# Kernel optimization log

Measured on AMD Instinct MI355X. Metric: run time of the kernel, lower is better.

Reference implementation:

```python
import jax, jax.numpy as jnp
import numpy as np

# Static layer configuration (from init_kwargs)
C_IN, H, W = 8, 32, 32
C_OUT, KH, KW = 16, 3, 3
SH, SW = 1, 1
PH, PW = 1, 1
OH = (H + 2 * PH - KH) // SH + 1
OW = (W + 2 * PW - KW) // SW + 1
N_IN = C_IN * H * W      # 8192 input-layer neurons
N_OUT = C_OUT * OH * OW  # 16384 output-layer neurons


def setup_inputs() -> dict:
    key = jax.random.key(0)
    k1, k2, k3, k4 = jax.random.split(key, 4)
    base = jax.random.normal(k1, (C_IN, H, W), dtype=jnp.float32)
    rad = jax.random.uniform(k2, (C_IN, H, W), dtype=jnp.float32)
    return {
        "concrete_lower": base - rad,   # ensure lower <= upper
        "concrete_upper": base + rad,
        "weights": jax.random.normal(k3, (C_OUT, C_IN, KH, KW), dtype=jnp.float32) * 0.1,
        "bias": jax.random.normal(k4, (C_OUT,), dtype=jnp.float32) * 0.1,
    }


def build_abstract_matrix(weights, bias):
    """Vectorized equivalent of _create_conv2d_channel_v0 over all channels.

    Produces M of shape (N_IN+1, N_OUT+1): column (c*OH*OW + i*OW + j) holds the
    affine coefficients (over flattened input neurons, bias in last row) of
    output pixel (c, i, j); last column is the homogeneous [0...0, 1] column.
    """
    idy = jnp.arange(OH)[:, None] * SH - PH + jnp.arange(KH)[None, :]  # (OH, KH)
    idx = jnp.arange(OW)[:, None] * SW - PW + jnp.arange(KW)[None, :]  # (OW, KW)
    valid = (((idy >= 0) & (idy < H))[:, :, None, None]
             & ((idx >= 0) & (idx < W))[None, None, :, :])             # (OH, KH, OW, KW)

    cin = jnp.arange(C_IN)
    # broadcast layout: (C_OUT, C_IN, OH, KH, OW, KW)
    rows = (cin[None, :, None, None, None, None] * (H * W)
            + idy[None, None, :, :, None, None] * W
            + idx[None, None, None, None, :, :])
    oc = jnp.arange(C_OUT)
    cols = (oc[:, None, None, None, None, None] * (OH * OW)
            + jnp.arange(OH)[None, None, :, None, None, None] * OW
            + jnp.arange(OW)[None, None, None, None, :, None])
    vals = weights[:, :, None, :, None, :]  # (C_OUT, C_IN, 1, KH, 1, KW)

    shape = (C_OUT, C_IN, OH, KH, OW, KW)
    rows_b = jnp.broadcast_to(rows, shape).reshape(-1)
    cols_b = jnp.broadcast_to(cols, shape).reshape(-1)
    vals_b = jnp.broadcast_to(vals, shape).reshape(-1)
    valid_b = jnp.broadcast_to(valid[None, None], shape).reshape(-1)
    # padding taps (out of input bounds) -> out-of-range row index, dropped by scatter
    rows_b = jnp.where(valid_b, rows_b, N_IN + 1)

    M = jnp.zeros((N_IN + 1, N_OUT + 1), dtype=jnp.float32)
    M = M.at[rows_b, cols_b].set(vals_b, mode="drop")
    M = M.at[N_IN, :N_OUT].set(jnp.repeat(bias, OH * OW))  # bias row per output pixel
    M = M.at[N_IN, N_OUT].set(1.0)                          # homogeneous corner
    return M


def back_substitute(M, l_in, u_in, lower=True):
    # Interval evaluation of the affine map: positive coeffs pair with one bound,
    # negative with the other; last row of M is the bias.
    Wc = M[:-1, :]
    b = M[-1, :]
    pos = jnp.maximum(Wc, 0.0)
    neg = jnp.minimum(Wc, 0.0)
    if lower:
        return l_in @ pos + u_in @ neg + b
    return u_in @ pos + l_in @ neg + b


def reference(concrete_lower, concrete_upper, weights, bias):
    M = build_abstract_matrix(weights, bias)  # abstract lower == upper for a conv layer
    l = concrete_lower.reshape(-1)
    u = concrete_upper.reshape(-1)
    lo = back_substitute(M, l, u, lower=True)[:N_OUT].reshape(C_OUT, OH, OW)
    hi = back_substitute(M, l, u, lower=False)[:N_OUT].reshape(C_OUT, OH, OW)
    return (lo, hi, M)
```

## Files before the change

kernel.cpp:

```cpp
#include <hip/hip_runtime.h>

#define C_IN  8
#define H     32
#define W     32
#define C_OUT 16
#define KH    3
#define KW    3
#define OH    32
#define OW    32
#define N_IN  (C_IN * H * W)
#define N_OUT (C_OUT * OH * OW)
#define MROWS (N_IN + 1)
#define MCOLS (N_OUT + 1)

__global__ __launch_bounds__(256) void build_M(const float* __restrict__ wts,
                                               const float* __restrict__ bias,
                                               float* __restrict__ M) {
    const int row = blockIdx.x;
    const int t   = threadIdx.x;
    float* __restrict__ Mrow = M + (size_t)row * MCOLS;

    if (row == N_IN) {
        for (int k = 0; k < 16; ++k) {
            float b = bias[k];
            float4 v = make_float4(b, b, b, b);
            *(float4*)(Mrow + 1024 * k + 4 * t) = v;
        }
        if (t == 0) Mrow[N_OUT] = 1.0f;
        return;
    }

    const int p    = (4 - (row & 3)) & 3;
    const int Nf   = (MCOLS - p) >> 2;
    const int tail = MCOLS - p - 4 * Nf;

    if (t < p)    Mrow[t] = 0.0f;
    if (t < tail) Mrow[p + 4 * Nf + t] = 0.0f;

    const float4 z = make_float4(0.0f, 0.0f, 0.0f, 0.0f);
    float* base = Mrow + p;
    #pragma unroll
    for (int k = 0; k < 16; ++k) {
        int idx = k * 256 + t;
        if (idx < Nf) *(float4*)(base + 4 * idx) = z;
    }

    const int cin = row >> 10;
    const int iy  = (row >> 5) & 31;
    const int ix  = row & 31;

    int   scol = -1;
    float wv   = 0.0f;
    if (t < C_OUT * KH * KW) {
        int c   = t / 9;
        int rem = t - 9 * c;
        int kh  = rem / 3;
        int kw  = rem - 3 * kh;
        int i   = iy + 1 - kh;
        int j   = ix + 1 - kw;
        if ((unsigned)i < 32u && (unsigned)j < 32u) {
            scol = c * 1024 + i * 32 + j;
            wv   = wts[c * 72 + cin * 9 + rem];
        }
    }

    __syncthreads();

    if (scol >= 0) Mrow[scol] = wv;
}

__global__ __launch_bounds__(256) void bounds_kernel(const float* __restrict__ l_in,
                                                     const float* __restrict__ u_in,
                                                     const float* __restrict__ wts,
                                                     const float* __restrict__ bias,
                                                     float* __restrict__ out) {
    int tid = blockIdx.x * 256 + threadIdx.x;
    if (tid >= N_OUT) return;
    int c = tid >> 10;
    int i = (tid >> 5) & 31;
    int j = tid & 31;

    float lo = bias[c];
    float hi = lo;

    #pragma unroll
    for (int cin = 0; cin < C_IN; ++cin) {
        #pragma unroll
        for (int kh = 0; kh < KH; ++kh) {
            int iy = i - 1 + kh;
            if ((unsigned)iy >= (unsigned)H) continue;
            #pragma unroll
            for (int kw = 0; kw < KW; ++kw) {
                int ix = j - 1 + kw;
                if ((unsigned)ix >= (unsigned)W) continue;
                float w = wts[c * 72 + cin * 9 + kh * 3 + kw];
                int   r = cin * 1024 + iy * 32 + ix;
                float a = w * l_in[r];
                float b = w * u_in[r];
                lo += fminf(a, b);
                hi += fmaxf(a, b);
            }
        }
    }
    out[tid]         = lo;
    out[N_OUT + tid] = hi;
}

extern "C" void kernel_launch(void* const* d_in, const int* in_sizes, int n_in,
                              void* d_out, int out_size, void* d_ws, size_t ws_size,
                              hipStream_t stream) {
    const float* lower = (const float*)d_in[0];
    const float* upper = (const float*)d_in[1];
    const float* wts   = (const float*)d_in[2];
    const float* bias  = (const float*)d_in[3];

    float* out = (float*)d_out;
    float* M   = out + 2 * N_OUT;

    hipLaunchKernelGGL(bounds_kernel, dim3((N_OUT + 255) / 256), dim3(256), 0, stream,
                       lower, upper, wts, bias, out);
    hipLaunchKernelGGL(build_M, dim3(MROWS), dim3(256), 0, stream, wts, bias, M);
}
```

Before: 571.1 us.

## Fuse bounds and matrix build into one kernel, computing M values in-register

Merges the bounds kernel and the M-construction kernel into a single launch, with the bounds work placed in trailing blocks. The M rows are no longer zero-filled first and then patched with scattered weight writes. Each thread now computes every element's value from weights staged in LDS and writes it in one float4 pass, which drops the barrier between fill and scatter and the separate launch. In exchange it adds per-element index arithmetic and LDS reads to a kernel bound by memory writes.

```diff
diff --git a/kernel.cpp b/kernel.cpp
--- a/kernel.cpp
+++ b/kernel.cpp
@@ -13,68 +13,97 @@
 #define MROWS (N_IN + 1)
 #define MCOLS (N_OUT + 1)
 
-__global__ __launch_bounds__(256) void build_M(const float* __restrict__ wts,
-                                               const float* __restrict__ bias,
-                                               float* __restrict__ M) {
-    const int row = blockIdx.x;
-    const int t   = threadIdx.x;
-    float* __restrict__ Mrow = M + (size_t)row * MCOLS;
+__global__ __launch_bounds__(256) void fused_kernel(const float* __restrict__ l_in,
+                                                    const float* __restrict__ u_in,
+                                                    const float* __restrict__ wts,
+                                                    const float* __restrict__ bias,
+                                                    float* __restrict__ out,
+                                                    float* __restrict__ M) {
+    const int b = blockIdx.x;
+    const int t = threadIdx.x;
 
-    if (row == N_IN) {
+    if (b < N_IN) {
+        const int row = b;
+        const int cin = row >> 10;
+        const int iy  = (row >> 5) & 31;
+        const int ix  = row & 31;
+
+        __shared__ float ldsW[160];
+        if (t < 144) {
+            int c = t / 9, r = t - 9 * c;
+            ldsW[t] = wts[c * 72 + cin * 9 + r];
+        } else if (t < 160) {
+            ldsW[t] = 0.0f;
+        }
+        __syncthreads();
+
+        float* __restrict__ Mrow = M + (size_t)row * MCOLS;
+        const int p    = (4 - (row & 3)) & 3;
+        const int Nf   = (MCOLS - p) >> 2;
+        const int tail = MCOLS - p - 4 * Nf;
+
+        if (t < p) {
+            int kh = iy + 1, kw = ix + 1 - t;
+            bool ok = ((unsigned)kh < 3u) & ((unsigned)kw < 3u);
+            Mrow[t] = ok ? ldsW[kh * 3 + kw] : 0.0f;
+        }
+        if (t < tail) {
+            int col = p + 4 * Nf + t;
+            float v = 0.0f;
+            if (col < N_OUT) {
+                int c = col >> 10, i = (col >> 5) & 31, j = col & 31;
+                int kh = iy + 1 - i, kw = ix + 1 - j;
+                if (((unsigned)kh < 3u) & ((unsigned)kw < 3u)) v = ldsW[c * 9 + kh * 3 + kw];
+            }
+            Mrow[col] = v;
+        }
+
+        int  add9[4];
+        bool okq[4];
+        int  klim[4];
+        const int e0 = p + 4 * t;
+        #pragma unroll
+        for (int q = 0; q < 4; ++q) {
+            int e     = e0 + q;
+            int carry = e >> 10;
+            int em    = e & 1023;
+            int i = em >> 5, j = em & 31;
+            int kh = iy + 1 - i, kw = ix + 1 - j;
+            bool ok = ((unsigned)kh < 3u) & ((unsigned)kw < 3u);
+            okq[q]  = ok;
+            add9[q] = carry * 9 + (ok ? kh * 3 + kw : 0);
+            klim[q] = 16 - carry;
+        }
+
+        float* dst = Mrow + p + 4 * t;
+        #pragma unroll
         for (int k = 0; k < 16; ++k) {
-            float b = bias[k];
-            float4 v = make_float4(b, b, b, b);
-            *(float4*)(Mrow + 1024 * k + 4 * t) = v;
+            int idx = (k << 8) + t;
+            if (idx < Nf) {
+                float vv[4];
+                #pragma unroll
+                for (int q = 0; q < 4; ++q) {
+                    float w = ldsW[k * 9 + add9[q]];
+                    vv[q] = (okq[q] & (k < klim[q])) ? w : 0.0f;
+                }
+                *(float4*)(dst + (k << 10)) = make_float4(vv[0], vv[1], vv[2], vv[3]);
+            }
+        }
+        return;
+    }
+
+    if (b == N_IN) {
+        float* __restrict__ Mrow = M + (size_t)N_IN * MCOLS;
+        #pragma unroll
+        for (int k = 0; k < 16; ++k) {
+            float bv = bias[k];
+            *(float4*)(Mrow + (k << 10) + 4 * t) = make_float4(bv, bv, bv, bv);
         }
         if (t == 0) Mrow[N_OUT] = 1.0f;
         return;
     }
 
-    const int p    = (4 - (row & 3)) & 3;
-    const int Nf   = (MCOLS - p) >> 2;
-    const int tail = MCOLS - p - 4 * Nf;
-
-    if (t < p)    Mrow[t] = 0.0f;
-    if (t < tail) Mrow[p + 4 * Nf + t] = 0.0f;
-
-    const float4 z = make_float4(0.0f, 0.0f, 0.0f, 0.0f);
-    float* base = Mrow + p;
-    #pragma unroll
-    for (int k = 0; k < 16; ++k) {
-        int idx = k * 256 + t;
-        if (idx < Nf) *(float4*)(base + 4 * idx) = z;
-    }
-
-    const int cin = row >> 10;
-    const int iy  = (row >> 5) & 31;
-    const int ix  = row & 31;
-
-    int   scol = -1;
-    float wv   = 0.0f;
-    if (t < C_OUT * KH * KW) {
-        int c   = t / 9;
-        int rem = t - 9 * c;
-        int kh  = rem / 3;
-        int kw  = rem - 3 * kh;
-        int i   = iy + 1 - kh;
-        int j   = ix + 1 - kw;
-        if ((unsigned)i < 32u && (unsigned)j < 32u) {
-            scol = c * 1024 + i * 32 + j;
-            wv   = wts[c * 72 + cin * 9 + rem];
-        }
-    }
-
-    __syncthreads();
-
-    if (scol >= 0) Mrow[scol] = wv;
-}
-
-__global__ __launch_bounds__(256) void bounds_kernel(const float* __restrict__ l_in,
-                                                     const float* __restrict__ u_in,
-                                                     const float* __restrict__ wts,
-                                                     const float* __restrict__ bias,
-                                                     float* __restrict__ out) {
-    int tid = blockIdx.x * 256 + threadIdx.x;
+    int tid = (b - (N_IN + 1)) * 256 + t;
     if (tid >= N_OUT) return;
     int c = tid >> 10;
     int i = (tid >> 5) & 31;
@@ -96,9 +125,9 @@
                 float w = wts[c * 72 + cin * 9 + kh * 3 + kw];
                 int   r = cin * 1024 + iy * 32 + ix;
                 float a = w * l_in[r];
-                float b = w * u_in[r];
-                lo += fminf(a, b);
-                hi += fmaxf(a, b);
+                float bb = w * u_in[r];
+                lo += fminf(a, bb);
+                hi += fmaxf(a, bb);
             }
         }
     }
@@ -117,7 +146,7 @@
     float* out = (float*)d_out;
     float* M   = out + 2 * N_OUT;
 
-    hipLaunchKernelGGL(bounds_kernel, dim3((N_OUT + 255) / 256), dim3(256), 0, stream,
-                       lower, upper, wts, bias, out);
-    hipLaunchKernelGGL(build_M, dim3(MROWS), dim3(256), 0, stream, wts, bias, M);
+    const int grid = N_IN + 1 + (N_OUT + 255) / 256;
+    hipLaunchKernelGGL(fused_kernel, dim3(grid), dim3(256), 0, stream,
+                       lower, upper, wts, bias, out, M);
 }
```

After: 558.2 us. 1.02x faster.
